# Performance work log

Measured on AMD Instinct MI355X. Metric: run time of the kernel, lower is better.

The kernel has to match this reference:

```python
import math
import jax, jax.numpy as jnp
import numpy as np

B, T, E, H = 4, 2048, 1024, 16
D = E // H          # head_dim = 64
F = D // 2          # num_pairs = 32
FREQ_SIGMA = 1.0


def _build_spiral_frequencies(num_heads, num_pairs, freq_sigma):
    indices = np.arange(num_pairs, dtype=np.float32) + 0.5
    magnitudes = np.linspace(freq_sigma / max(num_pairs, 1), freq_sigma, num_pairs, dtype=np.float32)
    head_phases = np.linspace(0.0, 2.0 * math.pi, num_heads + 1, dtype=np.float32)[:-1][:, None]
    golden = (1.0 + math.sqrt(5.0)) / 2.0
    y = np.clip(1.0 - 2.0 * indices / float(num_pairs), -1.0, 1.0)
    radius = np.sqrt(np.clip(1.0 - y ** 2, 0.0, None))
    theta = (2.0 * math.pi * indices / golden)[None, :] + head_phases
    x = radius[None, :] * np.cos(theta)
    z = radius[None, :] * np.sin(theta)
    directions = np.stack([x, np.broadcast_to(y[None, :], (num_heads, num_pairs)), z], axis=-1)
    return (directions * magnitudes[None, :, None]).astype(np.float32)  # (H, F, 3)


def setup_inputs() -> dict:
    key = jax.random.key(0)
    ks = jax.random.split(key, 4)
    query = jax.random.normal(ks[0], (B, T, E), dtype=jnp.float32)
    positions = jax.random.normal(ks[1], (B, T, 3), dtype=jnp.float32)
    in_proj_weight = jax.random.normal(ks[2], (3 * E, E), dtype=jnp.float32) * (1.0 / math.sqrt(E))
    in_proj_bias = jnp.zeros((3 * E,), dtype=jnp.float32)
    out_proj_weight = jax.random.normal(ks[3], (E, E), dtype=jnp.float32) * (1.0 / math.sqrt(E))
    out_proj_bias = jnp.zeros((E,), dtype=jnp.float32)
    freqs = jnp.asarray(_build_spiral_frequencies(H, F, FREQ_SIGMA))
    return dict(query=query, positions=positions, in_proj_weight=in_proj_weight,
                in_proj_bias=in_proj_bias, out_proj_weight=out_proj_weight,
                out_proj_bias=out_proj_bias, freqs=freqs)


def _apply_rotary(x, positions, freqs):
    # x: (B, H, T, D), positions: (B, T, 3), freqs: (H, F, 3)
    angles = jnp.einsum('btd,hfd->bhtf', positions.astype(jnp.float32), freqs.astype(jnp.float32))
    cos = jnp.cos(angles).astype(x.dtype)
    sin = jnp.sin(angles).astype(x.dtype)
    xr = x.reshape(*x.shape[:-1], F, 2)
    x0, x1 = xr[..., 0], xr[..., 1]
    rotated = jnp.stack((x0 * cos - x1 * sin, x0 * sin + x1 * cos), axis=-1)
    return rotated.reshape(x.shape)  # rotary_dim == head_dim here


def reference(query, positions, in_proj_weight, in_proj_bias, out_proj_weight, out_proj_bias, freqs):
    b, t, e = query.shape
    h = freqs.shape[0]
    d = e // h
    # QKV projections (self-attention: all from query)
    q = query @ in_proj_weight[:e].T + in_proj_bias[:e]
    k = query @ in_proj_weight[e:2 * e].T + in_proj_bias[e:2 * e]
    v = query @ in_proj_weight[2 * e:].T + in_proj_bias[2 * e:]
    # split heads -> (B, H, T, D)
    q = q.reshape(b, t, h, d).transpose(0, 2, 1, 3)
    k = k.reshape(b, t, h, d).transpose(0, 2, 1, 3)
    v = v.reshape(b, t, h, d).transpose(0, 2, 1, 3)
    q = _apply_rotary(q, positions, freqs)
    k = _apply_rotary(k, positions, freqs)
    # SDPA
    scale = 1.0 / math.sqrt(d)
    scores = jnp.einsum('bhqd,bhkd->bhqk', q, k) * scale
    attn = jax.nn.softmax(scores, axis=-1)
    out = jnp.einsum('bhqk,bhkd->bhqd', attn, v)
    out = out.transpose(0, 2, 1, 3).reshape(b, t, e)
    return out @ out_proj_weight.T + out_proj_bias
```

## Files before the change

kernel.cpp:

```cpp
#include <hip/hip_runtime.h>
#include <math.h>

#define NB 4
#define NT 2048
#define NE 1024
#define NH 16
#define ND 64
#define NF 32

typedef _Float16 half8 __attribute__((ext_vector_type(8)));
typedef __fp16 fp16x2 __attribute__((ext_vector_type(2)));
typedef unsigned int uint2v __attribute__((ext_vector_type(2)));
typedef unsigned int uint4v __attribute__((ext_vector_type(4)));
typedef float f32x4 __attribute__((ext_vector_type(4)));
typedef float f32x16 __attribute__((ext_vector_type(16)));
#define MFMA16(a, b, c) __builtin_amdgcn_mfma_f32_16x16x32_f16(a, b, c, 0, 0, 0)
#define MFMA32(a, b, c) __builtin_amdgcn_mfma_f32_32x32x16_f16(a, b, c, 0, 0, 0)

#define GLOAD_LDS16(gsrc, ldsbase)                                            \
    __builtin_amdgcn_global_load_lds(                                         \
        (const __attribute__((address_space(1))) void*)(gsrc),                \
        (__attribute__((address_space(3))) void*)(ldsbase), 16, 0, 0)

__device__ __forceinline__ float fast_exp2(float x) {
    float r;
    asm volatile("v_exp_f32 %0, %1" : "=v"(r) : "v"(x));
    return r;
}
__device__ __forceinline__ float max3f(float a, float b, float c) {
    return fmaxf(fmaxf(a, b), c);
}

__global__ __launch_bounds__(256)
void cvt_kernel(const float* __restrict__ X, const float* __restrict__ Wi,
                const float* __restrict__ Wo,
                _Float16* __restrict__ Xh, _Float16* __restrict__ Wih,
                _Float16* __restrict__ Woh)
{
    const size_t NX = (size_t)8388608, NWI = 3145728, NWO = 1048576;
    const size_t TOT = (NX + NWI + NWO) / 8;
    for (size_t gidx = (size_t)blockIdx.x*256 + threadIdx.x; gidx < TOT;
         gidx += (size_t)gridDim.x*256) {
        size_t i = gidx*8;
        const float* src; _Float16* dst; size_t off;
        if (i < NX)            { src = X;  dst = Xh;  off = i; }
        else if (i < NX + NWI) { src = Wi; dst = Wih; off = i - NX; }
        else                   { src = Wo; dst = Woh; off = i - NX - NWI; }
        float4 a = *(const float4*)(src + off);
        float4 b = *(const float4*)(src + off + 4);
        half8 h;
        h[0]=(_Float16)a.x; h[1]=(_Float16)a.y; h[2]=(_Float16)a.z; h[3]=(_Float16)a.w;
        h[4]=(_Float16)b.x; h[5]=(_Float16)b.y; h[6]=(_Float16)b.z; h[7]=(_Float16)b.w;
        *(half8*)(dst + off) = h;
    }
}

__global__ __launch_bounds__(256)
void qkv_mfma_kernel(const _Float16* __restrict__ Ah,
                     const _Float16* __restrict__ Bh,
                     const float* __restrict__ bias,
                     const float* __restrict__ pos,
                     const float* __restrict__ freqs,
                     _Float16* __restrict__ Qh,
                     _Float16* __restrict__ Kh,
                     _Float16* __restrict__ Vh)
{
    __shared__ _Float16 Ash[2][128*32];
    __shared__ _Float16 Bsh[2][128*32];

    const int tid = threadIdx.x;
    const int wid = tid >> 6, lane = tid & 63;
    const int ln = lane & 15, g = lane >> 4;
    const int wrow = wid >> 1, wcol = wid & 1;
    const int m0 = blockIdx.x * 128, n0 = blockIdx.y * 128;

    const int r0 = tid >> 2, s0 = tid & 3;
    const int k8 = s0 ^ ((r0 >> 1) & 3);
    const _Float16* gA0 = Ah + (size_t)(m0 + r0)      * NE + k8*8;
    const _Float16* gA1 = Ah + (size_t)(m0 + r0 + 64) * NE + k8*8;
    const _Float16* gB0 = Bh + (size_t)(n0 + r0)      * NE + k8*8;
    const _Float16* gB1 = Bh + (size_t)(n0 + r0 + 64) * NE + k8*8;

    const int wb = (tid & ~63) * 8;
    const int xr = g ^ ((ln >> 1) & 3);

    f32x4 acc[4][4];
    #pragma unroll
    for (int i = 0; i < 4; ++i)
        #pragma unroll
        for (int j = 0; j < 4; ++j) acc[i][j] = (f32x4){0.f,0.f,0.f,0.f};

    GLOAD_LDS16(gA0, Ash[0] + wb);
    GLOAD_LDS16(gA1, Ash[0] + wb + 256*8);
    GLOAD_LDS16(gB0, Bsh[0] + wb);
    GLOAD_LDS16(gB1, Bsh[0] + wb + 256*8);
    __syncthreads();

    for (int kt = 0; kt < NE; kt += 32) {
        const int cur = (kt >> 5) & 1;
        const int nxt = cur ^ 1;
        const int kn = kt + 32;
        if (kn < NE) {
            GLOAD_LDS16(gA0 + kn, Ash[nxt] + wb);
            GLOAD_LDS16(gA1 + kn, Ash[nxt] + wb + 256*8);
            GLOAD_LDS16(gB0 + kn, Bsh[nxt] + wb);
            GLOAD_LDS16(gB1 + kn, Bsh[nxt] + wb + 256*8);
        }
        half8 af[4], bf[4];
        #pragma unroll
        for (int mf = 0; mf < 4; ++mf)
            af[mf] = *(const half8*)&Ash[cur][(wrow*64 + mf*16 + ln)*32 + xr*8];
        #pragma unroll
        for (int nf = 0; nf < 4; ++nf)
            bf[nf] = *(const half8*)&Bsh[cur][(wcol*64 + nf*16 + ln)*32 + xr*8];
        __builtin_amdgcn_s_setprio(1);
        #pragma unroll
        for (int mf = 0; mf < 4; ++mf)
            #pragma unroll
            for (int nf = 0; nf < 4; ++nf)
                acc[mf][nf] = MFMA16(af[mf], bf[nf], acc[mf][nf]);
        __builtin_amdgcn_s_setprio(0);
        __syncthreads();
    }

    const int sec = n0 >> 10;
    _Float16* dst = (sec == 0) ? Qh : (sec == 1) ? Kh : Vh;

    float cb[4], fx[4], fy[4], fz[4];
    int hh[4], dd[4];
    #pragma unroll
    for (int nf = 0; nf < 4; ++nf) {
        const int col = n0 + wcol*64 + nf*16 + ln;
        cb[nf] = bias[col];
        const int e = col & 1023;
        hh[nf] = e >> 6; dd[nf] = e & 63;
        if (sec != 2) {
            const float* fq = freqs + ((size_t)hh[nf]*NF + (dd[nf] >> 1))*3;
            fx[nf] = fq[0]; fy[nf] = fq[1]; fz[nf] = fq[2];
        }
    }
    const float sgn = (ln & 1) ? 1.0f : -1.0f;
    const float qs  = (sec == 0) ? 0.125f * 1.4426950408889634f : 1.0f;

    #pragma unroll
    for (int mf = 0; mf < 4; ++mf) {
        #pragma unroll
        for (int r = 0; r < 4; ++r) {
            const int m = m0 + wrow*64 + mf*16 + g*4 + r;
            const int b = m >> 11, t = m & 2047;
            if (sec == 2) {
                #pragma unroll
                for (int nf = 0; nf < 4; ++nf)
                    dst[((size_t)(b*NH + hh[nf])*NT + t)*ND + dd[nf]] =
                        (_Float16)(acc[mf][nf][r] + cb[nf]);
            } else {
                const float px = pos[(size_t)m*3 + 0];
                const float py = pos[(size_t)m*3 + 1];
                const float pz = pos[(size_t)m*3 + 2];
                #pragma unroll
                for (int nf = 0; nf < 4; ++nf) {
                    const float x  = acc[mf][nf][r] + cb[nf];
                    const float xo = __shfl_xor(x, 1);
                    const float ang = px*fx[nf] + py*fy[nf] + pz*fz[nf];
                    float sn, cs;
                    __sincosf(ang, &sn, &cs);
                    const float out = (x*cs + sgn*xo*sn) * qs;
                    dst[((size_t)(b*NH + hh[nf])*NT + t)*ND + dd[nf]] = (_Float16)out;
                }
            }
        }
    }
}

__global__ __launch_bounds__(512, 4)
void attn_mfma_kernel(const _Float16* __restrict__ Qg, const _Float16* __restrict__ Kg,
                      const _Float16* __restrict__ Vg, _Float16* __restrict__ Og)
{
    __shared__ _Float16 Ks[2][64][70];
    __shared__ _Float16 VsT[2][64][70];

    const int tid  = threadIdx.x;
    const int wid  = tid >> 6;
    const int lane = tid & 63;
    const int m31  = lane & 31;
    const int hi   = lane >> 5;
    const int bh   = blockIdx.x;
    const int qt   = blockIdx.y;
    const int b = bh >> 4, h = bh & 15;
    const _Float16* Qp = Qg + (size_t)bh * NT * ND;
    const _Float16* Kp = Kg + (size_t)bh * NT * ND;
    const _Float16* Vp = Vg + (size_t)bh * NT * ND;

    const int qrow_g = qt*256 + wid*32 + m31;

    half8 qfr[4];
    #pragma unroll
    for (int c = 0; c < 4; ++c)
        qfr[c] = *(const half8*)(Qp + (size_t)qrow_g*ND + 16*c + 8*hi);

    f32x16 o0, o1;
    #pragma unroll
    for (int e = 0; e < 16; ++e) { o0[e] = 0.f; o1[e] = 0.f; }
    float m_i = 8.0f, l_i = 0.0f;

    const int sr  = tid >> 3;
    const int sc0 = (tid & 7) * 8;
    const int dp  = tid & 31;
    const int wv  = tid >> 5;
    const _Float16* kbase = Kp + (size_t)sr*ND + sc0;
    const _Float16* vbase = Vp + (size_t)(wv*4)*ND + 2*dp;

    half8 kv;
    unsigned int vr[4];

    #define LOADREGS(off)  do {                                              \
        kv = *(const half8*)(kbase + (size_t)(off)*ND);                      \
        _Pragma("unroll")                                                    \
        for (int j = 0; j < 4; ++j)                                          \
            vr[j] = *(const unsigned int*)(vbase + (size_t)((off) + j)*ND);  \
    } while (0)

    #define STOREBUF(bf)  do {                                               \
        *(half8*)&Ks[bf][sr][sc0] = kv;                                      \
        uint2v lod, hid;                                                     \
        lod[0] = __builtin_amdgcn_perm(vr[1], vr[0], 0x05040100u);           \
        lod[1] = __builtin_amdgcn_perm(vr[3], vr[2], 0x05040100u);           \
        hid[0] = __builtin_amdgcn_perm(vr[1], vr[0], 0x07060302u);           \
        hid[1] = __builtin_amdgcn_perm(vr[3], vr[2], 0x07060302u);           \
        *(uint2v*)&VsT[bf][2*dp][wv*4]     = lod;                            \
        *(uint2v*)&VsT[bf][2*dp + 1][wv*4] = hid;                            \
    } while (0)

    LOADREGS(0);
    STOREBUF(0);
    LOADREGS(64);

    for (int t = 0; t < 32; ++t) {
        const int cur = t & 1;
        __syncthreads();
        if (t < 31) STOREBUF(cur ^ 1);
        if (t < 30) LOADREGS((t + 2) * 64);

        f32x16 st0, st1;
        const float mneg = -m_i;
        #pragma unroll
        for (int e = 0; e < 16; ++e) { st0[e] = mneg; st1[e] = mneg; }

        __builtin_amdgcn_s_setprio(1);
        #pragma unroll
        for (int c = 0; c < 4; ++c) {
            half8 kf0 = *(const half8*)&Ks[cur][m31][16*c + 8*hi];
            half8 kf1 = *(const half8*)&Ks[cur][32 + m31][16*c + 8*hi];
            st0 = MFMA32(kf0, qfr[c], st0);
            st1 = MFMA32(kf1, qfr[c], st1);
        }
        __builtin_amdgcn_s_setprio(0);

        const fp16x2 ones2 = {(__fp16)1.0f, (__fp16)1.0f};
        unsigned int pku0[8], pku1[8];
        float rsA = 0.f, rsB = 0.f;
        float pmax = 0.f;
        #pragma unroll
        for (int j = 0; j < 8; ++j) {
            const float pa0 = fast_exp2(st0[2*j]);
            const float pa1 = fast_exp2(st0[2*j + 1]);
            const float pb0 = fast_exp2(st1[2*j]);
            const float pb1 = fast_exp2(st1[2*j + 1]);
            const fp16x2 h2a = __builtin_amdgcn_cvt_pkrtz(pa0, pa1);
            const fp16x2 h2b = __builtin_amdgcn_cvt_pkrtz(pb0, pb1);
            pku0[j] = __builtin_bit_cast(unsigned int, h2a);
            pku1[j] = __builtin_bit_cast(unsigned int, h2b);
            rsA = __builtin_amdgcn_fdot2(h2a, ones2, rsA, false);
            rsB = __builtin_amdgcn_fdot2(h2b, ones2, rsB, false);
            pmax = max3f(pmax, pa0, pa1);
            pmax = max3f(pmax, pb0, pb1);
        }
        float rs = rsA + rsB;
        rs += __shfl_xor(rs, 32);

        if (__any(pmax > 1.0f)) {
            pmax = fmaxf(pmax, __shfl_xor(pmax, 32));
            const bool  grow  = pmax > 1.0f;
            const float delta = grow ? log2f(pmax) : 0.0f;
            const float alpha = grow ? __builtin_amdgcn_rcpf(pmax) : 1.0f;
            m_i += delta;
            l_i *= alpha;
            rs  *= alpha;
            fp16x2 am; am[0] = (__fp16)alpha; am[1] = (__fp16)alpha;
            #pragma unroll
            for (int j = 0; j < 8; ++j) {
                fp16x2 p0v = __builtin_bit_cast(fp16x2, pku0[j]) * am;
                fp16x2 p1v = __builtin_bit_cast(fp16x2, pku1[j]) * am;
                pku0[j] = __builtin_bit_cast(unsigned int, p0v);
                pku1[j] = __builtin_bit_cast(unsigned int, p1v);
            }
            #pragma unroll
            for (int reg = 0; reg < 16; ++reg) {
                const int qr = (reg & 3) + 8*(reg >> 2) + 4*hi;
                const float a = __shfl(alpha, qr);
                o0[reg] *= a; o1[reg] *= a;
            }
        }
        l_i += rs;

        __builtin_amdgcn_s_setprio(1);
        #pragma unroll
        for (int kc = 0; kc < 4; ++kc) {
            const unsigned int a0 = (kc < 2) ? pku0[4*(kc & 1) + 0] : pku1[4*(kc & 1) + 0];
            const unsigned int a1 = (kc < 2) ? pku0[4*(kc & 1) + 1] : pku1[4*(kc & 1) + 1];
            const unsigned int b0 = (kc < 2) ? pku0[4*(kc & 1) + 2] : pku1[4*(kc & 1) + 2];
            const unsigned int b1 = (kc < 2) ? pku0[4*(kc & 1) + 3] : pku1[4*(kc & 1) + 3];
            uint2v rpa = __builtin_amdgcn_permlane32_swap(a0, b0, false, false);
            uint2v rpb = __builtin_amdgcn_permlane32_swap(a1, b1, false, false);
            uint4v u;
            u[0] = rpa[0]; u[1] = rpb[0]; u[2] = rpa[1]; u[3] = rpb[1];
            const half8 pa = __builtin_bit_cast(half8, u);
            const half8 vb0 = *(const half8*)&VsT[cur][m31][16*kc + 8*hi];
            const half8 vb1 = *(const half8*)&VsT[cur][32 + m31][16*kc + 8*hi];
            o0 = MFMA32(pa, vb0, o0);
            o1 = MFMA32(pa, vb1, o1);
        }
        __builtin_amdgcn_s_setprio(0);
    }

    #pragma unroll
    for (int reg = 0; reg < 16; ++reg) {
        const int qr = (reg & 3) + 8*(reg >> 2) + 4*hi;
        const float lq  = __shfl(l_i, qr);
        const float inv = 1.0f / lq;
        const int qg = qt*256 + wid*32 + qr;
        _Float16* dstp = Og + ((size_t)b*NT + qg)*NE + h*ND;
        dstp[m31]      = (_Float16)(o0[reg] * inv);
        dstp[32 + m31] = (_Float16)(o1[reg] * inv);
    }
    #undef LOADREGS
    #undef STOREBUF
}

__global__ __launch_bounds__(256)
void out_proj_mfma_kernel(const _Float16* __restrict__ Ah,
                          const _Float16* __restrict__ Bh,
                          const float* __restrict__ bias,
                          float* __restrict__ out)
{
    __shared__ _Float16 Ash[2][128*32];
    __shared__ _Float16 Bsh[2][128*32];

    const int tid = threadIdx.x;
    const int wid = tid >> 6, lane = tid & 63;
    const int ln = lane & 15, g = lane >> 4;
    const int wrow = wid >> 1, wcol = wid & 1;
    const int m0 = blockIdx.x * 128, n0 = blockIdx.y * 128;

    const int r0 = tid >> 2, s0 = tid & 3;
    const int k8 = s0 ^ ((r0 >> 1) & 3);
    const _Float16* gA0 = Ah + (size_t)(m0 + r0)      * NE + k8*8;
    const _Float16* gA1 = Ah + (size_t)(m0 + r0 + 64) * NE + k8*8;
    const _Float16* gB0 = Bh + (size_t)(n0 + r0)      * NE + k8*8;
    const _Float16* gB1 = Bh + (size_t)(n0 + r0 + 64) * NE + k8*8;

    const int wb = (tid & ~63) * 8;
    const int xr = g ^ ((ln >> 1) & 3);

    f32x4 acc[4][4];
    #pragma unroll
    for (int i = 0; i < 4; ++i)
        #pragma unroll
        for (int j = 0; j < 4; ++j) acc[i][j] = (f32x4){0.f,0.f,0.f,0.f};

    GLOAD_LDS16(gA0, Ash[0] + wb);
    GLOAD_LDS16(gA1, Ash[0] + wb + 256*8);
    GLOAD_LDS16(gB0, Bsh[0] + wb);
    GLOAD_LDS16(gB1, Bsh[0] + wb + 256*8);
    __syncthreads();

    for (int kt = 0; kt < NE; kt += 32) {
        const int cur = (kt >> 5) & 1;
        const int nxt = cur ^ 1;
        const int kn = kt + 32;
        if (kn < NE) {
            GLOAD_LDS16(gA0 + kn, Ash[nxt] + wb);
            GLOAD_LDS16(gA1 + kn, Ash[nxt] + wb + 256*8);
            GLOAD_LDS16(gB0 + kn, Bsh[nxt] + wb);
            GLOAD_LDS16(gB1 + kn, Bsh[nxt] + wb + 256*8);
        }
        half8 af[4], bf[4];
        #pragma unroll
        for (int mf = 0; mf < 4; ++mf)
            af[mf] = *(const half8*)&Ash[cur][(wrow*64 + mf*16 + ln)*32 + xr*8];
        #pragma unroll
        for (int nf = 0; nf < 4; ++nf)
            bf[nf] = *(const half8*)&Bsh[cur][(wcol*64 + nf*16 + ln)*32 + xr*8];
        __builtin_amdgcn_s_setprio(1);
        #pragma unroll
        for (int mf = 0; mf < 4; ++mf)
            #pragma unroll
            for (int nf = 0; nf < 4; ++nf)
                acc[mf][nf] = MFMA16(af[mf], bf[nf], acc[mf][nf]);
        __builtin_amdgcn_s_setprio(0);
        __syncthreads();
    }

    float cb[4];
    #pragma unroll
    for (int nf = 0; nf < 4; ++nf) cb[nf] = bias[n0 + wcol*64 + nf*16 + ln];

    #pragma unroll
    for (int mf = 0; mf < 4; ++mf)
        #pragma unroll
        for (int r = 0; r < 4; ++r) {
            const int m = m0 + wrow*64 + mf*16 + g*4 + r;
            #pragma unroll
            for (int nf = 0; nf < 4; ++nf)
                out[(size_t)m*NE + n0 + wcol*64 + nf*16 + ln] = acc[mf][nf][r] + cb[nf];
        }
}

extern "C" void kernel_launch(void* const* d_in, const int* in_sizes, int n_in,
                              void* d_out, int out_size, void* d_ws, size_t ws_size,
                              hipStream_t stream)
{
    const float* X   = (const float*)d_in[0];
    const float* pos = (const float*)d_in[1];
    const float* Wi  = (const float*)d_in[2];
    const float* bi  = (const float*)d_in[3];
    const float* Wo  = (const float*)d_in[4];
    const float* bo  = (const float*)d_in[5];
    const float* fr  = (const float*)d_in[6];
    float* out = (float*)d_out;

    _Float16* Xh  = (_Float16*)d_ws;
    _Float16* Wih = Xh  + 8388608;
    _Float16* Woh = Wih + 3145728;
    _Float16* Qh  = Woh + 1048576;
    _Float16* Kh  = Qh  + 8388608;
    _Float16* Vh  = Kh  + 8388608;
    _Float16* Oh  = Vh  + 8388608;

    cvt_kernel          <<<3072, 256, 0, stream>>>(X, Wi, Wo, Xh, Wih, Woh);
    qkv_mfma_kernel     <<<dim3(64, 24), 256, 0, stream>>>(Xh, Wih, bi, pos, fr, Qh, Kh, Vh);
    attn_mfma_kernel    <<<dim3(64, 8), 512, 0, stream>>>(Qh, Kh, Vh, Oh);
    out_proj_mfma_kernel<<<dim3(64, 8),  256, 0, stream>>>(Oh, Woh, bo, out);
}
```

Measured before the change: 212.2 us.

## Remap block indices for XCD locality, shrink attention blocks, use score-max rescale

The QKV and out-projection GEMMs switch to a 1D grid whose blocks are spread in round-robin groups of 8, so that blocks sharing A/B tiles land on the same XCD and can reuse its L2. The attention kernel drops from 512 to 256 threads per block (128 query rows), doubling the grid to 1024 blocks. Each thread now stages twice as much K/V data per tile, and blocks are remapped so neighbouring heads spread across XCDs. The online-softmax rescale trigger changes from a per-element max check to a row-sum threshold, with the max taken directly from the scores. This removes the max3 work from the hot loop but could let fp16 probabilities grow larger before rescaling.

Measured after the change: 226.0 us. +6.5%, slower.

```diff
diff --git a/kernel.cpp b/kernel.cpp
--- a/kernel.cpp
+++ b/kernel.cpp
@@ -72,7 +72,9 @@
     const int wid = tid >> 6, lane = tid & 63;
     const int ln = lane & 15, g = lane >> 4;
     const int wrow = wid >> 1, wcol = wid & 1;
-    const int m0 = blockIdx.x * 128, n0 = blockIdx.y * 128;
+    const int lin = blockIdx.x;
+    const int nsw = (lin & 7) * 192 + (lin >> 3);
+    const int m0 = (nsw & 63) * 128, n0 = (nsw >> 6) * 128;
 
     const int r0 = tid >> 2, s0 = tid & 3;
     const int k8 = s0 ^ ((r0 >> 1) & 3);
@@ -172,7 +174,7 @@
     }
 }
 
-__global__ __launch_bounds__(512, 4)
+__global__ __launch_bounds__(256, 4)
 void attn_mfma_kernel(const _Float16* __restrict__ Qg, const _Float16* __restrict__ Kg,
                       const _Float16* __restrict__ Vg, _Float16* __restrict__ Og)
 {
@@ -184,14 +186,16 @@
     const int lane = tid & 63;
     const int m31  = lane & 31;
     const int hi   = lane >> 5;
-    const int bh   = blockIdx.x;
-    const int qt   = blockIdx.y;
+    const int lin = blockIdx.x;
+    const int j   = lin >> 3;
+    const int qt  = j & 15;
+    const int bh  = (j >> 4) * 8 + (lin & 7);
     const int b = bh >> 4, h = bh & 15;
     const _Float16* Qp = Qg + (size_t)bh * NT * ND;
     const _Float16* Kp = Kg + (size_t)bh * NT * ND;
     const _Float16* Vp = Vg + (size_t)bh * NT * ND;
 
-    const int qrow_g = qt*256 + wid*32 + m31;
+    const int qrow_g = qt*128 + wid*32 + m31;
 
     half8 qfr[4];
     #pragma unroll
@@ -203,32 +207,35 @@
     for (int e = 0; e < 16; ++e) { o0[e] = 0.f; o1[e] = 0.f; }
     float m_i = 8.0f, l_i = 0.0f;
 
-    const int sr  = tid >> 3;
-    const int sc0 = (tid & 7) * 8;
+    const int sr  = tid >> 2;
+    const int sc0 = (tid & 3) * 16;
     const int dp  = tid & 31;
     const int wv  = tid >> 5;
     const _Float16* kbase = Kp + (size_t)sr*ND + sc0;
-    const _Float16* vbase = Vp + (size_t)(wv*4)*ND + 2*dp;
-
-    half8 kv;
-    unsigned int vr[4];
+    const _Float16* vbase = Vp + (size_t)(wv*8)*ND + 2*dp;
+
+    half8 kv0, kv1;
+    unsigned int vr[8];
 
     #define LOADREGS(off)  do {                                              \
-        kv = *(const half8*)(kbase + (size_t)(off)*ND);                      \
+        kv0 = *(const half8*)(kbase + (size_t)(off)*ND);                     \
+        kv1 = *(const half8*)(kbase + (size_t)(off)*ND + 8);                 \
         _Pragma("unroll")                                                    \
-        for (int j = 0; j < 4; ++j)                                          \
-            vr[j] = *(const unsigned int*)(vbase + (size_t)((off) + j)*ND);  \
+        for (int jj = 0; jj < 8; ++jj)                                       \
+            vr[jj] = *(const unsigned int*)(vbase + (size_t)((off) + jj)*ND);\
     } while (0)
 
     #define STOREBUF(bf)  do {                                               \
-        *(half8*)&Ks[bf][sr][sc0] = kv;                                      \
-        uint2v lod, hid;                                                     \
-        lod[0] = __builtin_amdgcn_perm(vr[1], vr[0], 0x05040100u);           \
-        lod[1] = __builtin_amdgcn_perm(vr[3], vr[2], 0x05040100u);           \
-        hid[0] = __builtin_amdgcn_perm(vr[1], vr[0], 0x07060302u);           \
-        hid[1] = __builtin_amdgcn_perm(vr[3], vr[2], 0x07060302u);           \
-        *(uint2v*)&VsT[bf][2*dp][wv*4]     = lod;                            \
-        *(uint2v*)&VsT[bf][2*dp + 1][wv*4] = hid;                            \
+        *(half8*)&Ks[bf][sr][sc0]     = kv0;                                 \
+        *(half8*)&Ks[bf][sr][sc0 + 8] = kv1;                                 \
+        uint4v lod, hid;                                                     \
+        _Pragma("unroll")                                                    \
+        for (int j2 = 0; j2 < 4; ++j2) {                                     \
+            lod[j2] = __builtin_amdgcn_perm(vr[2*j2+1], vr[2*j2], 0x05040100u); \
+            hid[j2] = __builtin_amdgcn_perm(vr[2*j2+1], vr[2*j2], 0x07060302u); \
+        }                                                                    \
+        *(uint4v*)&VsT[bf][2*dp][wv*8]     = lod;                            \
+        *(uint4v*)&VsT[bf][2*dp + 1][wv*8] = hid;                            \
     } while (0)
 
     LOADREGS(0);
@@ -259,40 +266,41 @@
         const fp16x2 ones2 = {(__fp16)1.0f, (__fp16)1.0f};
         unsigned int pku0[8], pku1[8];
         float rsA = 0.f, rsB = 0.f;
-        float pmax = 0.f;
-        #pragma unroll
-        for (int j = 0; j < 8; ++j) {
-            const float pa0 = fast_exp2(st0[2*j]);
-            const float pa1 = fast_exp2(st0[2*j + 1]);
-            const float pb0 = fast_exp2(st1[2*j]);
-            const float pb1 = fast_exp2(st1[2*j + 1]);
+        #pragma unroll
+        for (int jx = 0; jx < 8; ++jx) {
+            const float pa0 = fast_exp2(st0[2*jx]);
+            const float pa1 = fast_exp2(st0[2*jx + 1]);
+            const float pb0 = fast_exp2(st1[2*jx]);
+            const float pb1 = fast_exp2(st1[2*jx + 1]);
             const fp16x2 h2a = __builtin_amdgcn_cvt_pkrtz(pa0, pa1);
             const fp16x2 h2b = __builtin_amdgcn_cvt_pkrtz(pb0, pb1);
-            pku0[j] = __builtin_bit_cast(unsigned int, h2a);
-            pku1[j] = __builtin_bit_cast(unsigned int, h2b);
+            pku0[jx] = __builtin_bit_cast(unsigned int, h2a);
+            pku1[jx] = __builtin_bit_cast(unsigned int, h2b);
             rsA = __builtin_amdgcn_fdot2(h2a, ones2, rsA, false);
             rsB = __builtin_amdgcn_fdot2(h2b, ones2, rsB, false);
-            pmax = max3f(pmax, pa0, pa1);
-            pmax = max3f(pmax, pb0, pb1);
         }
         float rs = rsA + rsB;
         rs += __shfl_xor(rs, 32);
 
-        if (__any(pmax > 1.0f)) {
-            pmax = fmaxf(pmax, __shfl_xor(pmax, 32));
-            const bool  grow  = pmax > 1.0f;
-            const float delta = grow ? log2f(pmax) : 0.0f;
-            const float alpha = grow ? __builtin_amdgcn_rcpf(pmax) : 1.0f;
+        if (__any(rs > 256.0f)) {
+            float smax = st0[0];
+            #pragma unroll
+            for (int e = 1; e < 16; ++e) smax = fmaxf(smax, st0[e]);
+            #pragma unroll
+            for (int e = 0; e < 16; ++e) smax = fmaxf(smax, st1[e]);
+            smax = fmaxf(smax, __shfl_xor(smax, 32));
+            const float delta = (smax > 0.0f) ? smax : 0.0f;
+            const float alpha = fast_exp2(-delta);
             m_i += delta;
             l_i *= alpha;
             rs  *= alpha;
             fp16x2 am; am[0] = (__fp16)alpha; am[1] = (__fp16)alpha;
             #pragma unroll
-            for (int j = 0; j < 8; ++j) {
-                fp16x2 p0v = __builtin_bit_cast(fp16x2, pku0[j]) * am;
-                fp16x2 p1v = __builtin_bit_cast(fp16x2, pku1[j]) * am;
-                pku0[j] = __builtin_bit_cast(unsigned int, p0v);
-                pku1[j] = __builtin_bit_cast(unsigned int, p1v);
+            for (int jx = 0; jx < 8; ++jx) {
+                fp16x2 p0v = __builtin_bit_cast(fp16x2, pku0[jx]) * am;
+                fp16x2 p1v = __builtin_bit_cast(fp16x2, pku1[jx]) * am;
+                pku0[jx] = __builtin_bit_cast(unsigned int, p0v);
+                pku1[jx] = __builtin_bit_cast(unsigned int, p1v);
             }
             #pragma unroll
             for (int reg = 0; reg < 16; ++reg) {
@@ -328,7 +336,7 @@
         const int qr = (reg & 3) + 8*(reg >> 2) + 4*hi;
         const float lq  = __shfl(l_i, qr);
         const float inv = 1.0f / lq;
-        const int qg = qt*256 + wid*32 + qr;
+        const int qg = qt*128 + wid*32 + qr;
         _Float16* dstp = Og + ((size_t)b*NT + qg)*NE + h*ND;
         dstp[m31]      = (_Float16)(o0[reg] * inv);
         dstp[32 + m31] = (_Float16)(o1[reg] * inv);
@@ -350,7 +358,9 @@
     const int wid = tid >> 6, lane = tid & 63;
     const int ln = lane & 15, g = lane >> 4;
     const int wrow = wid >> 1, wcol = wid & 1;
-    const int m0 = blockIdx.x * 128, n0 = blockIdx.y * 128;
+    const int lin = blockIdx.x;
+    const int nsw = (lin & 7) * 64 + (lin >> 3);
+    const int m0 = (nsw & 63) * 128, n0 = (nsw >> 6) * 128;
 
     const int r0 = tid >> 2, s0 = tid & 3;
     const int k8 = s0 ^ ((r0 >> 1) & 3);
@@ -438,7 +448,7 @@
     _Float16* Oh  = Vh  + 8388608;
 
     cvt_kernel          <<<3072, 256, 0, stream>>>(X, Wi, Wo, Xh, Wih, Woh);
-    qkv_mfma_kernel     <<<dim3(64, 24), 256, 0, stream>>>(Xh, Wih, bi, pos, fr, Qh, Kh, Vh);
-    attn_mfma_kernel    <<<dim3(64, 8), 512, 0, stream>>>(Qh, Kh, Vh, Oh);
-    out_proj_mfma_kernel<<<dim3(64, 8),  256, 0, stream>>>(Oh, Woh, bo, out);
-}
+    qkv_mfma_kernel     <<<1536, 256, 0, stream>>>(Xh, Wih, bi, pos, fr, Qh, Kh, Vh);
+    attn_mfma_kernel    <<<1024, 256, 0, stream>>>(Qh, Kh, Vh, Oh);
+    out_proj_mfma_kernel<<<512,  256, 0, stream>>>(Oh, Woh, bo, out);
+}
```
